# Kernel optimization log

Measured on AMD Instinct MI355X. Metric: run time of the kernel, lower is better.

Reference implementation:

```python
import jax, jax.numpy as jnp
import numpy as np

NEG_SLOPE = 0.2


def gat_conv(h, src, dst, n_dst, W_src, W_dst, attn_l, attn_r, bias):
    # h: [N_src, F_in]; edges src->dst; dst nodes are a prefix of src nodes.
    H, D = attn_l.shape
    z_src = (h @ W_src).reshape(h.shape[0], H, D)          # [N_src, H, D]
    z_dst = (h[:n_dst] @ W_dst).reshape(n_dst, H, D)       # [N_dst, H, D]
    el = jnp.einsum('nhd,hd->nh', z_src, attn_l)           # [N_src, H]
    er = jnp.einsum('nhd,hd->nh', z_dst, attn_r)           # [N_dst, H]
    e = jax.nn.leaky_relu(el[src] + er[dst], NEG_SLOPE)    # [E, H]
    # numerically stable edge softmax over incoming edges of each dst node
    m = jax.ops.segment_max(e, dst, num_segments=n_dst)    # [N_dst, H]
    w = jnp.exp(e - m[dst])                                # [E, H]
    s = jax.ops.segment_sum(w, dst, num_segments=n_dst)    # [N_dst, H]
    alpha = w / s[dst]                                     # [E, H]
    msg = alpha[:, :, None] * z_src[src]                   # [E, H, D]
    out = jax.ops.segment_sum(msg, dst, num_segments=n_dst)
    return out + bias                                      # [N_dst, H, D]


def setup_inputs() -> dict:
    key = jax.random.key(0)
    ks = jax.random.split(key, 16)
    IN, HID, HEADS, NCLS = 256, 64, 4, 47
    N_SRC0, N_DST0, E0 = 200000, 50000, 500000
    N_DST1, E1 = 10000, 100000
    sc0 = 0.1
    inp = {
        'x': jax.random.normal(ks[0], (N_SRC0, IN), jnp.float32),
        'src0': jax.random.randint(ks[1], (E0,), 0, N_SRC0, jnp.int32),
        'dst0': jax.random.randint(ks[2], (E0,), 0, N_DST0, jnp.int32),
        'src1': jax.random.randint(ks[3], (E1,), 0, N_DST0, jnp.int32),
        'dst1': jax.random.randint(ks[4], (E1,), 0, N_DST1, jnp.int32),
        'num_dst0': N_DST0,
        'num_dst1': N_DST1,
        'W0_src': jax.random.normal(ks[5], (IN, HEADS * HID), jnp.float32) * sc0,
        'W0_dst': jax.random.normal(ks[6], (IN, HEADS * HID), jnp.float32) * sc0,
        'attn_l0': jax.random.normal(ks[7], (HEADS, HID), jnp.float32) * sc0,
        'attn_r0': jax.random.normal(ks[8], (HEADS, HID), jnp.float32) * sc0,
        'bias0': jnp.zeros((HEADS, HID), jnp.float32),
        'W1_src': jax.random.normal(ks[9], (HEADS * HID, HEADS * NCLS), jnp.float32) * sc0,
        'W1_dst': jax.random.normal(ks[10], (HEADS * HID, HEADS * NCLS), jnp.float32) * sc0,
        'attn_l1': jax.random.normal(ks[11], (HEADS, NCLS), jnp.float32) * sc0,
        'attn_r1': jax.random.normal(ks[12], (HEADS, NCLS), jnp.float32) * sc0,
        'bias1': jnp.zeros((HEADS, NCLS), jnp.float32),
    }
    return inp


def reference(x, src0, dst0, src1, dst1, num_dst0, num_dst1,
              W0_src, W0_dst, attn_l0, attn_r0, bias0,
              W1_src, W1_dst, attn_l1, attn_r1, bias1):
    # layer 0: GATConv + relu activation, flatten heads
    h = gat_conv(x, src0, dst0, num_dst0, W0_src, W0_dst, attn_l0, attn_r0, bias0)
    h = jax.nn.relu(h).reshape(num_dst0, -1)               # [N_dst0, H*HID]
    # layer 1: GATConv, no activation
    h = gat_conv(h, src1, dst1, num_dst1, W1_src, W1_dst, attn_l1, attn_r1, bias1)
    h = h.mean(axis=1)                                     # mean over heads -> [N_dst1, n_classes]
    return jax.nn.log_softmax(h, axis=-1)
```

## Files before the change

### kernel.cpp

```cpp
#include <hip/hip_runtime.h>
#include <math.h>

typedef _Float16 half8 __attribute__((ext_vector_type(8)));
typedef _Float16 half4 __attribute__((ext_vector_type(4)));
typedef float f32x4 __attribute__((ext_vector_type(4)));

constexpr int IN    = 256;
constexpr int HEADS = 4;
constexpr int HID   = 64;
constexpr int NCLS  = 47;
constexpr int HD0   = 256;
constexpr int HD1   = 188;
constexpr float NEG_SLOPE = 0.2f;
constexpr int ND0 = 50000, ND1 = 10000;

static __device__ __forceinline__ float leaky(float x) {
    return x >= 0.f ? x : NEG_SLOPE * x;
}

__device__ __forceinline__ void gload16(const void* g, void* l) {
    __builtin_amdgcn_global_load_lds((const __attribute__((address_space(1))) void*)g,
                                     (__attribute__((address_space(3))) void*)l, 16, 0, 0);
}

__global__ void make_vT(const float* __restrict__ W, const float* __restrict__ attn,
                        float* __restrict__ vT, int D) {
    int id = blockIdx.x * blockDim.x + threadIdx.x;
    if (id >= IN * HEADS) return;
    int k = id >> 2, h = id & 3;
    const float* wr = W + (size_t)k * (HEADS * D) + h * D;
    const float* ar = attn + h * D;
    float s = 0.f;
    for (int d = 0; d < D; ++d) s += wr[d] * ar[d];
    vT[h * IN + k] = s;
}

__global__ void cvtB(const float* __restrict__ W, _Float16* __restrict__ Bt, int N, int BROWS) {
    int id = blockIdx.x * 256 + threadIdx.x;
    if (id >= BROWS * IN) return;
    int n = id / IN, k = id % IN;
    Bt[id] = (n < N) ? (_Float16)W[(size_t)k * N + n] : (_Float16)0.f;
}

template <bool AHALF, int BCOLS, int NOUT, bool ZHALF, int FEL>
__global__ __launch_bounds__(512) void gemm_stream(const void* __restrict__ Av,
        const _Float16* __restrict__ Bt, void* __restrict__ Z,
        const float* __restrict__ attn_flat, float* __restrict__ el, int M) {
    constexpr int FN = BCOLS / 16;
    __shared__ __align__(16) _Float16 Bs[BCOLS * 256];
    const int t = threadIdx.x;
    const int l = t & 63, w = t >> 6;
    const int lr = l & 15, lh = l >> 4;

    constexpr int ITERS = (BCOLS * 32) / 512;
#pragma unroll
    for (int it = 0; it < ITERS; ++it) {
        int c = it * 512 + t;
        int r = c >> 5, s = c & 31;
        int cs = s ^ (((r & 15) << 1) ^ ((r >> 4) & 1));
        gload16(Bt + (size_t)r * IN + cs * 8, (char*)Bs + (it * 512 + w * 64) * 16);
    }
    __syncthreads();

    const int R0 = blockIdx.x * 128 + w * 16;
    int arow = R0 + lr; if (arow >= M) arow = M - 1;

    f32x4 acc[FN];
#pragma unroll
    for (int nj = 0; nj < FN; ++nj) {
        acc[nj][0] = 0.f; acc[nj][1] = 0.f; acc[nj][2] = 0.f; acc[nj][3] = 0.f;
    }

    half8 av[8];
    float4 a0[8], a1[8];
    if constexpr (AHALF) {
        const _Float16* ap = (const _Float16*)Av + (size_t)arow * IN + lh * 8;
#pragma unroll
        for (int tt = 0; tt < 8; ++tt) av[tt] = *(const half8*)(ap + tt * 32);
    } else {
        const float* ap = (const float*)Av + (size_t)arow * IN + lh * 8;
#pragma unroll
        for (int tt = 0; tt < 8; ++tt) {
            a0[tt] = *(const float4*)(ap + tt * 32);
            a1[tt] = *(const float4*)(ap + tt * 32 + 4);
        }
    }

    const int swz_l = lr << 1;
#pragma unroll
    for (int tt = 0; tt < 8; ++tt) {
        half8 af;
        if constexpr (AHALF) {
            af = av[tt];
        } else {
            af[0] = (_Float16)a0[tt].x; af[1] = (_Float16)a0[tt].y;
            af[2] = (_Float16)a0[tt].z; af[3] = (_Float16)a0[tt].w;
            af[4] = (_Float16)a1[tt].x; af[5] = (_Float16)a1[tt].y;
            af[6] = (_Float16)a1[tt].z; af[7] = (_Float16)a1[tt].w;
        }
#pragma unroll
        for (int nj = 0; nj < FN; ++nj) {
            int colr = nj * 16 + lr;
            int slot = (tt * 4 + lh) ^ swz_l ^ (nj & 1);
            half8 bf = *(const half8*)&Bs[colr * 256 + slot * 8];
            acc[nj] = __builtin_amdgcn_mfma_f32_16x16x32_f16(af, bf, acc[nj], 0, 0, 0);
        }
    }

#pragma unroll
    for (int r = 0; r < 4; ++r) {
        int grow = R0 + lh * 4 + r;
        if (grow < M) {
#pragma unroll
            for (int nj = 0; nj < FN; ++nj) {
                int col = nj * 16 + lr;
                if (col < NOUT) {
                    if constexpr (ZHALF)
                        ((_Float16*)Z)[(size_t)grow * NOUT + col] = (_Float16)acc[nj][r];
                    else
                        ((float*)Z)[(size_t)grow * NOUT + col] = acc[nj][r];
                }
            }
        }
    }

    if constexpr (FEL > 0) {
        float alv[FN];
#pragma unroll
        for (int nj = 0; nj < FN; ++nj) {
            int col = nj * 16 + lr;
            if constexpr (FEL == 1) alv[nj] = attn_flat[col];
            else                    alv[nj] = (col < NOUT) ? attn_flat[col] : 0.f;
        }
#pragma unroll
        for (int r = 0; r < 4; ++r) {
            float sh0 = 0.f, sh1 = 0.f, sh2 = 0.f, sh3 = 0.f;
#pragma unroll
            for (int nj = 0; nj < FN; ++nj) {
                float v = acc[nj][r] * alv[nj];
                if constexpr (FEL == 1) {
                    if constexpr (true) {
                        switch (nj >> 2) {
                            case 0: sh0 += v; break;
                            case 1: sh1 += v; break;
                            case 2: sh2 += v; break;
                            default: sh3 += v; break;
                        }
                    }
                } else {
                    int col = nj * 16 + lr;
                    int hs = col < 47 ? 0 : col < 94 ? 1 : col < 141 ? 2 : 3;
                    sh0 += (hs == 0) ? v : 0.f;
                    sh1 += (hs == 1) ? v : 0.f;
                    sh2 += (hs == 2) ? v : 0.f;
                    sh3 += (hs == 3) ? v : 0.f;
                }
            }
#pragma unroll
            for (int off = 1; off <= 8; off <<= 1) {
                sh0 += __shfl_xor(sh0, off); sh1 += __shfl_xor(sh1, off);
                sh2 += __shfl_xor(sh2, off); sh3 += __shfl_xor(sh3, off);
            }
            int grow = R0 + lh * 4 + r;
            if (lr == 0 && grow < M)
                *(float4*)(el + (size_t)grow * 4) = make_float4(sh0, sh1, sh2, sh3);
        }
    }
}

__global__ __launch_bounds__(256) void gemv_er_f32(const float* __restrict__ A,
        const float* __restrict__ vrT, float* __restrict__ er, int M) {
    int wv = threadIdx.x >> 6, lane = threadIdx.x & 63;
    int row = blockIdx.x * 4 + wv;
    if (row >= M) return;
    float4 xa = *(const float4*)(A + (size_t)row * IN + lane * 4);
    float s[4];
#pragma unroll
    for (int h = 0; h < 4; ++h) {
        float4 v = *(const float4*)(vrT + h * IN + lane * 4);
        s[h] = xa.x * v.x + xa.y * v.y + xa.z * v.z + xa.w * v.w;
    }
#pragma unroll
    for (int off = 32; off; off >>= 1)
#pragma unroll
        for (int h = 0; h < 4; ++h) s[h] += __shfl_xor(s[h], off);
    if (lane == 0) *(float4*)(er + (size_t)row * 4) = make_float4(s[0], s[1], s[2], s[3]);
}

__global__ __launch_bounds__(256) void gemv_er_f16(const _Float16* __restrict__ A,
        const float* __restrict__ vrT, float* __restrict__ er, int M) {
    int wv = threadIdx.x >> 6, lane = threadIdx.x & 63;
    int row = blockIdx.x * 4 + wv;
    if (row >= M) return;
    half4 ah = *(const half4*)(A + (size_t)row * IN + lane * 4);
    float a0 = (float)ah[0], a1 = (float)ah[1], a2 = (float)ah[2], a3 = (float)ah[3];
    float s[4];
#pragma unroll
    for (int h = 0; h < 4; ++h) {
        float4 v = *(const float4*)(vrT + h * IN + lane * 4);
        s[h] = a0 * v.x + a1 * v.y + a2 * v.z + a3 * v.w;
    }
#pragma unroll
    for (int off = 32; off; off >>= 1)
#pragma unroll
        for (int h = 0; h < 4; ++h) s[h] += __shfl_xor(s[h], off);
    if (lane == 0) *(float4*)(er + (size_t)row * 4) = make_float4(s[0], s[1], s[2], s[3]);
}

__global__ void hist_k(const int* __restrict__ dst, int E, int* __restrict__ counts) {
    int i = blockIdx.x * blockDim.x + threadIdx.x;
    if (i < E) atomicAdd(&counts[dst[i]], 1);
}

__global__ __launch_bounds__(256) void scan1_k(const int* __restrict__ counts, int n,
                                               int* __restrict__ part) {
    __shared__ int ws[4];
    int i = blockIdx.x * 256 + threadIdx.x;
    int lane = threadIdx.x & 63, wv = threadIdx.x >> 6;
    int s = (i < n) ? counts[i] : 0;
#pragma unroll
    for (int off = 32; off; off >>= 1) s += __shfl_xor(s, off);
    if (lane == 0) ws[wv] = s;
    __syncthreads();
    if (threadIdx.x == 0) part[blockIdx.x] = ws[0] + ws[1] + ws[2] + ws[3];
}

__global__ __launch_bounds__(256) void scan2_k(int* __restrict__ part, int nb) {
    __shared__ int ws[4];
    int tid = threadIdx.x, lane = tid & 63, wv = tid >> 6;
    int v = (tid < nb) ? part[tid] : 0;
    int x = v;
#pragma unroll
    for (int off = 1; off < 64; off <<= 1) {
        int u = __shfl_up(x, off);
        if (lane >= off) x += u;
    }
    if (lane == 63) ws[wv] = x;
    __syncthreads();
    int base = 0;
    for (int k = 0; k < wv; ++k) base += ws[k];
    if (tid < nb) part[tid] = base + x - v;
}

__global__ __launch_bounds__(256) void scan3_k(const int* __restrict__ counts, int n,
        const int* __restrict__ part, int* __restrict__ offsets, int* __restrict__ cursor) {
    __shared__ int ws[4];
    int i = blockIdx.x * 256 + threadIdx.x;
    int lane = threadIdx.x & 63, wv = threadIdx.x >> 6;
    int v = (i < n) ? counts[i] : 0;
    int x = v;
#pragma unroll
    for (int off = 1; off < 64; off <<= 1) {
        int u = __shfl_up(x, off);
        if (lane >= off) x += u;
    }
    if (lane == 63) ws[wv] = x;
    __syncthreads();
    int base = part[blockIdx.x];
    for (int k = 0; k < wv; ++k) base += ws[k];
    int off_ = base + x - v;
    if (i < n) { offsets[i] = off_; cursor[i] = off_; }
    if (i == n - 1) offsets[n] = off_ + v;
}

__global__ void scatter_k(const int* __restrict__ src, const int* __restrict__ dst, int E,
        int* __restrict__ cursor, int* __restrict__ ssrc) {
    int i = blockIdx.x * blockDim.x + threadIdx.x;
    if (i < E) {
        int p = atomicAdd(&cursor[dst[i]], 1);
        ssrc[p] = src[i];
    }
}

__global__ __launch_bounds__(256) void agg_l0(const int* __restrict__ ssrc,
        const int* __restrict__ offs, const float* __restrict__ el,
        const float* __restrict__ er, const _Float16* __restrict__ z,
        const float* __restrict__ bias, _Float16* __restrict__ h, int nd) {
    int wv = threadIdx.x >> 6, lane = threadIdx.x & 63;
    int d = blockIdx.x * 4 + wv;
    if (d >= nd) return;
    int head = lane >> 4;
    int beg = offs[d], end = offs[d + 1];
    float erh = er[(size_t)d * 4 + head];
    float ax = 0, ay = 0, az = 0, aw = 0, ssum = 0;
    for (int j0 = beg; j0 < end; j0 += 64) {
        int nn = min(64, end - j0);
        int myidx = (lane < nn) ? ssrc[j0 + lane] : 0;
        for (int j = 0; j < nn; ++j) {
            int s = __shfl(myidx, j);
            float e = el[(size_t)s * 4 + head] + erh;
            float wgt = __expf(leaky(e));
            ssum += wgt;
            half4 zv = *(const half4*)(z + (size_t)s * HD0 + lane * 4);
            ax += wgt * (float)zv[0]; ay += wgt * (float)zv[1];
            az += wgt * (float)zv[2]; aw += wgt * (float)zv[3];
        }
    }
    float inv = ssum > 0.f ? 1.f / ssum : 0.f;
    const float* b = bias + lane * 4;
    half4 o;
    o[0] = (_Float16)fmaxf(ax * inv + b[0], 0.f);
    o[1] = (_Float16)fmaxf(ay * inv + b[1], 0.f);
    o[2] = (_Float16)fmaxf(az * inv + b[2], 0.f);
    o[3] = (_Float16)fmaxf(aw * inv + b[3], 0.f);
    *(half4*)(h + (size_t)d * HD0 + lane * 4) = o;
}

__global__ __launch_bounds__(256) void agg_l1(const int* __restrict__ ssrc,
        const int* __restrict__ offs, const float* __restrict__ el,
        const float* __restrict__ er, const float* __restrict__ z,
        const float* __restrict__ bias, float* __restrict__ out, int nd) {
    int wv = threadIdx.x >> 6, lane = threadIdx.x & 63;
    int d = blockIdx.x * 4 + wv;
    if (d >= nd) return;
    int beg = offs[d], end = offs[d + 1];
    float4 er4 = *(const float4*)(er + (size_t)d * 4);
    const int f0 = lane, f1 = lane + 64, f2 = lane + 128;
    const int h0 = f0 / NCLS, h1 = f1 / NCLS;
    const bool has2 = f2 < HD1;
    const int h2 = has2 ? f2 / NCLS : 3;
    float a0 = 0, a1 = 0, a2 = 0;
    float s0 = 0, s1 = 0, s2 = 0, s3 = 0;
    for (int j0 = beg; j0 < end; j0 += 64) {
        int nn = min(64, end - j0);
        int myidx = (lane < nn) ? ssrc[j0 + lane] : 0;
        for (int j = 0; j < nn; ++j) {
            int s = __shfl(myidx, j);
            float4 e4 = *(const float4*)(el + (size_t)s * 4);
            float w0 = __expf(leaky(e4.x + er4.x));
            float w1 = __expf(leaky(e4.y + er4.y));
            float w2 = __expf(leaky(e4.z + er4.z));
            float w3 = __expf(leaky(e4.w + er4.w));
            s0 += w0; s1 += w1; s2 += w2; s3 += w3;
            const float* zr = z + (size_t)s * HD1;
            a0 += (h0 == 0 ? w0 : h0 == 1 ? w1 : h0 == 2 ? w2 : w3) * zr[f0];
            a1 += (h1 == 0 ? w0 : h1 == 1 ? w1 : h1 == 2 ? w2 : w3) * zr[f1];
            if (has2) a2 += (h2 == 0 ? w0 : h2 == 1 ? w1 : h2 == 2 ? w2 : w3) * zr[f2];
        }
    }
    float sa = h0 == 0 ? s0 : h0 == 1 ? s1 : h0 == 2 ? s2 : s3;
    float sb = h1 == 0 ? s0 : h1 == 1 ? s1 : h1 == 2 ? s2 : s3;
    float sc = h2 == 0 ? s0 : h2 == 1 ? s1 : h2 == 2 ? s2 : s3;
    float* orow = out + (size_t)d * HD1;
    orow[f0] = a0 * (sa > 0.f ? 1.f / sa : 0.f) + bias[f0];
    orow[f1] = a1 * (sb > 0.f ? 1.f / sb : 0.f) + bias[f1];
    if (has2) orow[f2] = a2 * (sc > 0.f ? 1.f / sc : 0.f) + bias[f2];
}

__global__ __launch_bounds__(256) void final_k(const float* __restrict__ o1,
        float* __restrict__ y, int n) {
    int wave = threadIdx.x >> 6, lane = threadIdx.x & 63;
    int node = blockIdx.x * 4 + wave;
    if (node >= n) return;
    const float* r = o1 + (size_t)node * HD1;
    float vv = 0.f, v = -INFINITY;
    if (lane < NCLS) {
        vv = 0.25f * (r[lane] + r[lane + NCLS] + r[lane + 2 * NCLS] + r[lane + 3 * NCLS]);
        v = vv;
    }
    float mx = v;
#pragma unroll
    for (int off = 32; off; off >>= 1) mx = fmaxf(mx, __shfl_xor(mx, off));
    float p = (lane < NCLS) ? __expf(vv - mx) : 0.f;
    float sum = p;
#pragma unroll
    for (int off = 32; off; off >>= 1) sum += __shfl_xor(sum, off);
    if (lane < NCLS) y[(size_t)node * NCLS + lane] = vv - mx - logf(sum);
}

extern "C" void kernel_launch(void* const* d_in, const int* in_sizes, int n_in,
                              void* d_out, int out_size, void* d_ws, size_t ws_size,
                              hipStream_t stream) {
    const float* x    = (const float*)d_in[0];
    const int*   src0 = (const int*)d_in[1];
    const int*   dst0 = (const int*)d_in[2];
    const int*   src1 = (const int*)d_in[3];
    const int*   dst1 = (const int*)d_in[4];
    const float* W0s  = (const float*)d_in[7];
    const float* W0d  = (const float*)d_in[8];
    const float* al0  = (const float*)d_in[9];
    const float* ar0  = (const float*)d_in[10];
    const float* b0   = (const float*)d_in[11];
    const float* W1s  = (const float*)d_in[12];
    const float* W1d  = (const float*)d_in[13];
    const float* al1  = (const float*)d_in[14];
    const float* ar1  = (const float*)d_in[15];
    const float* b1   = (const float*)d_in[16];
    const int E0 = in_sizes[1], E1 = in_sizes[3];
    const int NS0 = in_sizes[0] / IN;

    char* p = (char*)d_ws;
    auto take = [&](size_t bytes) {
        char* r = p;
        p += (bytes + 255) & ~(size_t)255;
        return r;
    };
    _Float16* z0  = (_Float16*)take((size_t)NS0 * HD0 * 2);
    _Float16* h   = (_Float16*)take((size_t)ND0 * HD0 * 2);
    float*    z1  = (float*)take((size_t)ND0 * HD1 * 4);
    float*    o1  = (float*)take((size_t)ND1 * HD1 * 4);
    float*    el0 = (float*)take((size_t)NS0 * 4 * 4);
    float*    er0 = (float*)take((size_t)ND0 * 4 * 4);
    float*    el1 = (float*)take((size_t)ND0 * 4 * 4);
    float*    er1 = (float*)take((size_t)ND1 * 4 * 4);
    _Float16* B0t = (_Float16*)take((size_t)256 * IN * 2);
    _Float16* B1t = (_Float16*)take((size_t)192 * IN * 2);
    float*    vr0T = (float*)take(4 * IN * 4);
    float*    vr1T = (float*)take(4 * IN * 4);
    int* counts0 = (int*)take((size_t)ND0 * 4);
    int* offs0   = (int*)take((size_t)(ND0 + 1) * 4);
    int* cur0    = (int*)take((size_t)ND0 * 4);
    int* ss0     = (int*)take((size_t)E0 * 4);
    int* counts1 = (int*)take((size_t)ND1 * 4);
    int* offs1   = (int*)take((size_t)(ND1 + 1) * 4);
    int* cur1    = (int*)take((size_t)ND1 * 4);
    int* ss1     = (int*)take((size_t)E1 * 4);
    int* part0   = (int*)take(256 * 4);
    int* part1   = (int*)take(256 * 4);

    const int NB0 = (ND0 + 255) / 256, NB1 = (ND1 + 255) / 256;

    hipMemsetAsync(counts0, 0, (size_t)ND0 * 4, stream);
    hipMemsetAsync(counts1, 0, (size_t)ND1 * 4, stream);

    make_vT<<<4, 256, 0, stream>>>(W0d, ar0, vr0T, HID);
    make_vT<<<4, 256, 0, stream>>>(W1d, ar1, vr1T, NCLS);
    cvtB<<<256, 256, 0, stream>>>(W0s, B0t, HD0, 256);
    cvtB<<<192, 256, 0, stream>>>(W1s, B1t, HD1, 192);

    gemm_stream<false, 256, 256, true, 1><<<(NS0 + 127) / 128, 512, 0, stream>>>(
        (const void*)x, B0t, (void*)z0, al0, el0, NS0);
    gemv_er_f32<<<(ND0 + 3) / 4, 256, 0, stream>>>(x, vr0T, er0, ND0);
    hist_k<<<(E0 + 255) / 256, 256, 0, stream>>>(dst0, E0, counts0);
    scan1_k<<<NB0, 256, 0, stream>>>(counts0, ND0, part0);
    scan2_k<<<1, 256, 0, stream>>>(part0, NB0);
    scan3_k<<<NB0, 256, 0, stream>>>(counts0, ND0, part0, offs0, cur0);
    scatter_k<<<(E0 + 255) / 256, 256, 0, stream>>>(src0, dst0, E0, cur0, ss0);
    agg_l0<<<(ND0 + 3) / 4, 256, 0, stream>>>(ss0, offs0, el0, er0, z0, b0, h, ND0);

    gemm_stream<true, 192, 188, false, 2><<<(ND0 + 127) / 128, 512, 0, stream>>>(
        (const void*)h, B1t, (void*)z1, al1, el1, ND0);
    gemv_er_f16<<<(ND1 + 3) / 4, 256, 0, stream>>>(h, vr1T, er1, ND1);
    hist_k<<<(E1 + 255) / 256, 256, 0, stream>>>(dst1, E1, counts1);
    scan1_k<<<NB1, 256, 0, stream>>>(counts1, ND1, part1);
    scan2_k<<<1, 256, 0, stream>>>(part1, NB1);
    scan3_k<<<NB1, 256, 0, stream>>>(counts1, ND1, part1, offs1, cur1);
    scatter_k<<<(E1 + 255) / 256, 256, 0, stream>>>(src1, dst1, E1, cur1, ss1);
    agg_l1<<<(ND1 + 3) / 4, 256, 0, stream>>>(ss1, offs1, el1, er1, z1, b1, o1, ND1);

    final_k<<<(ND1 + 3) / 4, 256, 0, stream>>>(o1, (float*)d_out, ND1);
}
```

Measured before the change: 333.1 us.

## Make GEMM persistent with double-buffered A loads; unroll aggregation edge loops

The projection GEMM becomes a persistent kernel with a grid of 256 blocks that loops over 128-row tiles. It keeps the B matrix in LDS once per block and prefetches the next tile's A rows into registers while computing the current one, so global-load latency overlaps MFMA work and the per-block B reload is paid less often. The layer-0 and layer-1 aggregation loops are also unrolled by 4 and 2 edges to put more independent gathers in flight. The costs are much higher register pressure from two A buffers (launch bounds ask for 2 blocks per CU), possible spills, and fewer blocks to hide latency.

New measurement: 381.0 us. 14.4% more time.

```diff
diff --git a/kernel.cpp b/kernel.cpp
--- a/kernel.cpp
+++ b/kernel.cpp
@@ -43,14 +43,15 @@
 }
 
 template <bool AHALF, int BCOLS, int NOUT, bool ZHALF, int FEL>
-__global__ __launch_bounds__(512) void gemm_stream(const void* __restrict__ Av,
+__global__ __launch_bounds__(512, 2) void gemm_persist(const void* __restrict__ Av,
         const _Float16* __restrict__ Bt, void* __restrict__ Z,
-        const float* __restrict__ attn_flat, float* __restrict__ el, int M) {
+        const float* __restrict__ attn_flat, float* __restrict__ el, int M, int ntiles) {
     constexpr int FN = BCOLS / 16;
     __shared__ __align__(16) _Float16 Bs[BCOLS * 256];
     const int t = threadIdx.x;
     const int l = t & 63, w = t >> 6;
     const int lr = l & 15, lh = l >> 4;
+    const int G = gridDim.x;
 
     constexpr int ITERS = (BCOLS * 32) / 512;
 #pragma unroll
@@ -62,109 +63,124 @@
     }
     __syncthreads();
 
-    const int R0 = blockIdx.x * 128 + w * 16;
-    int arow = R0 + lr; if (arow >= M) arow = M - 1;
-
-    f32x4 acc[FN];
-#pragma unroll
-    for (int nj = 0; nj < FN; ++nj) {
-        acc[nj][0] = 0.f; acc[nj][1] = 0.f; acc[nj][2] = 0.f; acc[nj][3] = 0.f;
-    }
-
-    half8 av[8];
-    float4 a0[8], a1[8];
-    if constexpr (AHALF) {
-        const _Float16* ap = (const _Float16*)Av + (size_t)arow * IN + lh * 8;
-#pragma unroll
-        for (int tt = 0; tt < 8; ++tt) av[tt] = *(const half8*)(ap + tt * 32);
-    } else {
-        const float* ap = (const float*)Av + (size_t)arow * IN + lh * 8;
-#pragma unroll
-        for (int tt = 0; tt < 8; ++tt) {
-            a0[tt] = *(const float4*)(ap + tt * 32);
-            a1[tt] = *(const float4*)(ap + tt * 32 + 4);
-        }
-    }
-
-    const int swz_l = lr << 1;
-#pragma unroll
-    for (int tt = 0; tt < 8; ++tt) {
-        half8 af;
-        if constexpr (AHALF) {
-            af = av[tt];
-        } else {
-            af[0] = (_Float16)a0[tt].x; af[1] = (_Float16)a0[tt].y;
-            af[2] = (_Float16)a0[tt].z; af[3] = (_Float16)a0[tt].w;
-            af[4] = (_Float16)a1[tt].x; af[5] = (_Float16)a1[tt].y;
-            af[6] = (_Float16)a1[tt].z; af[7] = (_Float16)a1[tt].w;
-        }
-#pragma unroll
-        for (int nj = 0; nj < FN; ++nj) {
-            int colr = nj * 16 + lr;
-            int slot = (tt * 4 + lh) ^ swz_l ^ (nj & 1);
-            half8 bf = *(const half8*)&Bs[colr * 256 + slot * 8];
-            acc[nj] = __builtin_amdgcn_mfma_f32_16x16x32_f16(af, bf, acc[nj], 0, 0, 0);
-        }
-    }
-
-#pragma unroll
-    for (int r = 0; r < 4; ++r) {
-        int grow = R0 + lh * 4 + r;
-        if (grow < M) {
-#pragma unroll
-            for (int nj = 0; nj < FN; ++nj) {
-                int col = nj * 16 + lr;
-                if (col < NOUT) {
-                    if constexpr (ZHALF)
-                        ((_Float16*)Z)[(size_t)grow * NOUT + col] = (_Float16)acc[nj][r];
-                    else
-                        ((float*)Z)[(size_t)grow * NOUT + col] = acc[nj][r];
-                }
-            }
-        }
-    }
-
+    float alv[FN];
     if constexpr (FEL > 0) {
-        float alv[FN];
 #pragma unroll
         for (int nj = 0; nj < FN; ++nj) {
             int col = nj * 16 + lr;
             if constexpr (FEL == 1) alv[nj] = attn_flat[col];
             else                    alv[nj] = (col < NOUT) ? attn_flat[col] : 0.f;
         }
+    }
+
+    float4 fA0[8], fA1[8], fB0[8], fB1[8];
+    half8  hA[8], hB[8];
+
+    auto issue = [&](int tile, float4 (&x0)[8], float4 (&x1)[8], half8 (&xh)[8]) {
+        int row = tile * 128 + w * 16 + lr;
+        if (row >= M) row = M - 1;
+        if constexpr (AHALF) {
+            const _Float16* ap = (const _Float16*)Av + (size_t)row * IN + lh * 8;
+#pragma unroll
+            for (int tt = 0; tt < 8; ++tt) xh[tt] = *(const half8*)(ap + tt * 32);
+        } else {
+            const float* ap = (const float*)Av + (size_t)row * IN + lh * 8;
+#pragma unroll
+            for (int tt = 0; tt < 8; ++tt) {
+                x0[tt] = *(const float4*)(ap + tt * 32);
+                x1[tt] = *(const float4*)(ap + tt * 32 + 4);
+            }
+        }
+        __builtin_amdgcn_sched_barrier(0);
+    };
+
+    const int swz_l = lr << 1;
+    auto compute_store = [&](int tile, float4 (&x0)[8], float4 (&x1)[8], half8 (&xh)[8]) {
+        f32x4 acc[FN];
+#pragma unroll
+        for (int nj = 0; nj < FN; ++nj) {
+            acc[nj][0] = 0.f; acc[nj][1] = 0.f; acc[nj][2] = 0.f; acc[nj][3] = 0.f;
+        }
+#pragma unroll
+        for (int tt = 0; tt < 8; ++tt) {
+            half8 af;
+            if constexpr (AHALF) {
+                af = xh[tt];
+            } else {
+                af[0] = (_Float16)x0[tt].x; af[1] = (_Float16)x0[tt].y;
+                af[2] = (_Float16)x0[tt].z; af[3] = (_Float16)x0[tt].w;
+                af[4] = (_Float16)x1[tt].x; af[5] = (_Float16)x1[tt].y;
+                af[6] = (_Float16)x1[tt].z; af[7] = (_Float16)x1[tt].w;
+            }
+#pragma unroll
+            for (int nj = 0; nj < FN; ++nj) {
+                int colr = nj * 16 + lr;
+                int slot = (tt * 4 + lh) ^ swz_l ^ (nj & 1);
+                half8 bf = *(const half8*)&Bs[colr * 256 + slot * 8];
+                acc[nj] = __builtin_amdgcn_mfma_f32_16x16x32_f16(af, bf, acc[nj], 0, 0, 0);
+            }
+        }
+        const int R0 = tile * 128 + w * 16;
 #pragma unroll
         for (int r = 0; r < 4; ++r) {
-            float sh0 = 0.f, sh1 = 0.f, sh2 = 0.f, sh3 = 0.f;
-#pragma unroll
-            for (int nj = 0; nj < FN; ++nj) {
-                float v = acc[nj][r] * alv[nj];
-                if constexpr (FEL == 1) {
-                    if constexpr (true) {
+            int grow = R0 + lh * 4 + r;
+            if (grow < M) {
+#pragma unroll
+                for (int nj = 0; nj < FN; ++nj) {
+                    int col = nj * 16 + lr;
+                    if (col < NOUT) {
+                        if constexpr (ZHALF)
+                            ((_Float16*)Z)[(size_t)grow * NOUT + col] = (_Float16)acc[nj][r];
+                        else
+                            ((float*)Z)[(size_t)grow * NOUT + col] = acc[nj][r];
+                    }
+                }
+            }
+        }
+        if constexpr (FEL > 0) {
+#pragma unroll
+            for (int r = 0; r < 4; ++r) {
+                float sh0 = 0.f, sh1 = 0.f, sh2 = 0.f, sh3 = 0.f;
+#pragma unroll
+                for (int nj = 0; nj < FN; ++nj) {
+                    float v = acc[nj][r] * alv[nj];
+                    if constexpr (FEL == 1) {
                         switch (nj >> 2) {
                             case 0: sh0 += v; break;
                             case 1: sh1 += v; break;
                             case 2: sh2 += v; break;
                             default: sh3 += v; break;
                         }
+                    } else {
+                        int col = nj * 16 + lr;
+                        int hs = col < 47 ? 0 : col < 94 ? 1 : col < 141 ? 2 : 3;
+                        sh0 += (hs == 0) ? v : 0.f;
+                        sh1 += (hs == 1) ? v : 0.f;
+                        sh2 += (hs == 2) ? v : 0.f;
+                        sh3 += (hs == 3) ? v : 0.f;
                     }
-                } else {
-                    int col = nj * 16 + lr;
-                    int hs = col < 47 ? 0 : col < 94 ? 1 : col < 141 ? 2 : 3;
-                    sh0 += (hs == 0) ? v : 0.f;
-                    sh1 += (hs == 1) ? v : 0.f;
-                    sh2 += (hs == 2) ? v : 0.f;
-                    sh3 += (hs == 3) ? v : 0.f;
                 }
+#pragma unroll
+                for (int off = 1; off <= 8; off <<= 1) {
+                    sh0 += __shfl_xor(sh0, off); sh1 += __shfl_xor(sh1, off);
+                    sh2 += __shfl_xor(sh2, off); sh3 += __shfl_xor(sh3, off);
+                }
+                int grow = R0 + lh * 4 + r;
+                if (lr == 0 && grow < M)
+                    *(float4*)(el + (size_t)grow * 4) = make_float4(sh0, sh1, sh2, sh3);
             }
-#pragma unroll
-            for (int off = 1; off <= 8; off <<= 1) {
-                sh0 += __shfl_xor(sh0, off); sh1 += __shfl_xor(sh1, off);
-                sh2 += __shfl_xor(sh2, off); sh3 += __shfl_xor(sh3, off);
-            }
-            int grow = R0 + lh * 4 + r;
-            if (lr == 0 && grow < M)
-                *(float4*)(el + (size_t)grow * 4) = make_float4(sh0, sh1, sh2, sh3);
-        }
+        }
+    };
+
+    int t0 = blockIdx.x;
+    if (t0 < ntiles) issue(t0, fA0, fA1, hA);
+    for (int tt0 = t0; tt0 < ntiles; tt0 += 2 * G) {
+        int t1 = tt0 + G;
+        if (t1 < ntiles) issue(t1, fB0, fB1, hB);
+        compute_store(tt0, fA0, fA1, hA);
+        int t2 = tt0 + 2 * G;
+        if (t2 < ntiles) issue(t2, fA0, fA1, hA);
+        if (t1 < ntiles) compute_store(t1, fB0, fB1, hB);
     }
 }
 
@@ -286,7 +302,25 @@
     for (int j0 = beg; j0 < end; j0 += 64) {
         int nn = min(64, end - j0);
         int myidx = (lane < nn) ? ssrc[j0 + lane] : 0;
-        for (int j = 0; j < nn; ++j) {
+        int j = 0;
+        for (; j + 4 <= nn; j += 4) {
+            int s0 = __shfl(myidx, j),     s1 = __shfl(myidx, j + 1);
+            int s2 = __shfl(myidx, j + 2), s3 = __shfl(myidx, j + 3);
+            float e0 = el[(size_t)s0 * 4 + head], e1 = el[(size_t)s1 * 4 + head];
+            float e2 = el[(size_t)s2 * 4 + head], e3 = el[(size_t)s3 * 4 + head];
+            half4 zv0 = *(const half4*)(z + (size_t)s0 * HD0 + lane * 4);
+            half4 zv1 = *(const half4*)(z + (size_t)s1 * HD0 + lane * 4);
+            half4 zv2 = *(const half4*)(z + (size_t)s2 * HD0 + lane * 4);
+            half4 zv3 = *(const half4*)(z + (size_t)s3 * HD0 + lane * 4);
+            float w0 = __expf(leaky(e0 + erh)), w1 = __expf(leaky(e1 + erh));
+            float w2 = __expf(leaky(e2 + erh)), w3 = __expf(leaky(e3 + erh));
+            ssum += (w0 + w1) + (w2 + w3);
+            ax += w0 * (float)zv0[0] + w1 * (float)zv1[0] + w2 * (float)zv2[0] + w3 * (float)zv3[0];
+            ay += w0 * (float)zv0[1] + w1 * (float)zv1[1] + w2 * (float)zv2[1] + w3 * (float)zv3[1];
+            az += w0 * (float)zv0[2] + w1 * (float)zv1[2] + w2 * (float)zv2[2] + w3 * (float)zv3[2];
+            aw += w0 * (float)zv0[3] + w1 * (float)zv1[3] + w2 * (float)zv2[3] + w3 * (float)zv3[3];
+        }
+        for (; j < nn; ++j) {
             int s = __shfl(myidx, j);
             float e = el[(size_t)s * 4 + head] + erh;
             float wgt = __expf(leaky(e));
@@ -324,7 +358,29 @@
     for (int j0 = beg; j0 < end; j0 += 64) {
         int nn = min(64, end - j0);
         int myidx = (lane < nn) ? ssrc[j0 + lane] : 0;
-        for (int j = 0; j < nn; ++j) {
+        int j = 0;
+        for (; j + 2 <= nn; j += 2) {
+            int sa_ = __shfl(myidx, j), sb_ = __shfl(myidx, j + 1);
+            float4 ea = *(const float4*)(el + (size_t)sa_ * 4);
+            float4 eb = *(const float4*)(el + (size_t)sb_ * 4);
+            const float* za = z + (size_t)sa_ * HD1;
+            const float* zb = z + (size_t)sb_ * HD1;
+            float za0 = za[f0], za1 = za[f1], za2 = has2 ? za[f2] : 0.f;
+            float zb0 = zb[f0], zb1 = zb[f1], zb2 = has2 ? zb[f2] : 0.f;
+            float wa0 = __expf(leaky(ea.x + er4.x)), wa1 = __expf(leaky(ea.y + er4.y));
+            float wa2 = __expf(leaky(ea.z + er4.z)), wa3 = __expf(leaky(ea.w + er4.w));
+            float wb0 = __expf(leaky(eb.x + er4.x)), wb1 = __expf(leaky(eb.y + er4.y));
+            float wb2 = __expf(leaky(eb.z + er4.z)), wb3 = __expf(leaky(eb.w + er4.w));
+            s0 += wa0 + wb0; s1 += wa1 + wb1; s2 += wa2 + wb2; s3 += wa3 + wb3;
+            a0 += (h0 == 0 ? wa0 : h0 == 1 ? wa1 : h0 == 2 ? wa2 : wa3) * za0
+                + (h0 == 0 ? wb0 : h0 == 1 ? wb1 : h0 == 2 ? wb2 : wb3) * zb0;
+            a1 += (h1 == 0 ? wa0 : h1 == 1 ? wa1 : h1 == 2 ? wa2 : wa3) * za1
+                + (h1 == 0 ? wb0 : h1 == 1 ? wb1 : h1 == 2 ? wb2 : wb3) * zb1;
+            if (has2)
+                a2 += (h2 == 0 ? wa0 : h2 == 1 ? wa1 : h2 == 2 ? wa2 : wa3) * za2
+                    + (h2 == 0 ? wb0 : h2 == 1 ? wb1 : h2 == 2 ? wb2 : wb3) * zb2;
+        }
+        for (; j < nn; ++j) {
             int s = __shfl(myidx, j);
             float4 e4 = *(const float4*)(el + (size_t)s * 4);
             float w0 = __expf(leaky(e4.x + er4.x));
@@ -419,6 +475,7 @@
     int* part1   = (int*)take(256 * 4);
 
     const int NB0 = (ND0 + 255) / 256, NB1 = (ND1 + 255) / 256;
+    const int NT0 = (NS0 + 127) / 128, NT1 = (ND0 + 127) / 128;
 
     hipMemsetAsync(counts0, 0, (size_t)ND0 * 4, stream);
     hipMemsetAsync(counts1, 0, (size_t)ND1 * 4, stream);
@@ -428,8 +485,8 @@
     cvtB<<<256, 256, 0, stream>>>(W0s, B0t, HD0, 256);
     cvtB<<<192, 256, 0, stream>>>(W1s, B1t, HD1, 192);
 
-    gemm_stream<false, 256, 256, true, 1><<<(NS0 + 127) / 128, 512, 0, stream>>>(
-        (const void*)x, B0t, (void*)z0, al0, el0, NS0);
+    gemm_persist<false, 256, 256, true, 1><<<256, 512, 0, stream>>>(
+        (const void*)x, B0t, (void*)z0, al0, el0, NS0, NT0);
     gemv_er_f32<<<(ND0 + 3) / 4, 256, 0, stream>>>(x, vr0T, er0, ND0);
     hist_k<<<(E0 + 255) / 256, 256, 0, stream>>>(dst0, E0, counts0);
     scan1_k<<<NB0, 256, 0, stream>>>(counts0, ND0, part0);
@@ -438,8 +495,8 @@
     scatter_k<<<(E0 + 255) / 256, 256, 0, stream>>>(src0, dst0, E0, cur0, ss0);
     agg_l0<<<(ND0 + 3) / 4, 256, 0, stream>>>(ss0, offs0, el0, er0, z0, b0, h, ND0);
 
-    gemm_stream<true, 192, 188, false, 2><<<(ND0 + 127) / 128, 512, 0, stream>>>(
-        (const void*)h, B1t, (void*)z1, al1, el1, ND0);
+    gemm_persist<true, 192, 188, false, 2><<<256, 512, 0, stream>>>(
+        (const void*)h, B1t, (void*)z1, al1, el1, ND0, NT1);
     gemv_er_f16<<<(ND1 + 3) / 4, 256, 0, stream>>>(h, vr1T, er1, ND1);
     hist_k<<<(E1 + 255) / 256, 256, 0, stream>>>(dst1, E1, counts1);
     scan1_k<<<NB1, 256, 0, stream>>>(counts1, ND1, part1);
```
